# Kernel tuning notes

Measured on AMD Instinct MI355X. Metric: run time of the kernel, lower is better.

Reference implementation:

```python
import jax, jax.numpy as jnp
import numpy as np

B, N, D, H, IN, HID = 16, 1024, 256, 8, 256, 1024
HD = IN // H  # head dim = 32
EPS = 1e-5


def layer_norm(x, g, b):
    mu = jnp.mean(x, axis=-1, keepdims=True)
    var = jnp.var(x, axis=-1, keepdims=True)
    return (x - mu) / jnp.sqrt(var + EPS) * g + b


def setup_inputs() -> dict:
    key = jax.random.key(0)
    ks = jax.random.split(key, 12)
    s = 0.02
    return {
        "x": jax.random.normal(ks[0], (B, N, D), jnp.float32),
        "coords": jax.random.normal(ks[1], (B, N, 2), jnp.float32),
        "g1": jnp.ones((D,), jnp.float32),
        "b1": jnp.zeros((D,), jnp.float32),
        "Wqkv": jax.random.normal(ks[2], (3 * IN, D), jnp.float32) * s,
        "Wproj": jax.random.normal(ks[3], (IN, IN), jnp.float32) * s,
        "bproj": jnp.zeros((IN,), jnp.float32),
        "g2": jnp.ones((D,), jnp.float32),
        "b2": jnp.zeros((D,), jnp.float32),
        "W1": jax.random.normal(ks[4], (HID, D), jnp.float32) * s,
        "bb1": jnp.zeros((HID,), jnp.float32),
        "W2": jax.random.normal(ks[5], (D, HID), jnp.float32) * s,
        "bb2": jnp.zeros((D,), jnp.float32),
    }


def reference(x, coords, g1, b1, Wqkv, Wproj, bproj, g2, b2, W1, bb1, W2, bb2):
    # ---- Attention branch (pre-norm) ----
    h = layer_norm(x, g1, b1)                       # [B,N,D]
    qkv = h @ Wqkv.T                                # [B,N,3*IN]
    qkv = qkv.reshape(B, N, 3, H, HD).transpose(2, 0, 3, 1, 4)  # [3,B,H,N,HD]
    q, k, v = qkv[0], qkv[1], qkv[2]
    scale = HD ** -0.5
    attn = jnp.einsum('bhid,bhjd->bhij', q * scale, k)  # [B,H,N,N]
    attn = jax.nn.softmax(attn, axis=-1)
    o = jnp.einsum('bhij,bhjd->bhid', attn, v)      # [B,H,N,HD]
    o = o.transpose(0, 2, 1, 3).reshape(B, N, IN)   # [B,N,IN]
    o = o @ Wproj.T + bproj
    o = o + h                                       # residual inside Attention (vs normed input)
    x = x + o                                       # Block residual (double residual, faithful)
    # ---- MLP branch ----
    h2 = layer_norm(x, g2, b2)
    m = jax.nn.gelu(h2 @ W1.T + bb1, approximate=False) @ W2.T + bb2
    return x + m
```

## Files before the change

### kernel.cpp

```cpp
#include <hip/hip_runtime.h>
#include <hip/hip_bf16.h>
#include <math.h>

#define Bdim 16
#define Ndim 1024
#define Ddim 256
#define Hdim 8
#define HDdim 32
#define INdim 256
#define HIDdim 1024
#define Tdim (Bdim * Ndim)

typedef __attribute__((ext_vector_type(8)))  short bf16x8;
typedef __attribute__((ext_vector_type(4)))  short bf16x4;
typedef __attribute__((ext_vector_type(16))) float f32x16;
typedef unsigned int u32;

__device__ inline short f2bf(float x) {
    union { __hip_bfloat16 b; short s; } u;
    u.b = __float2bfloat16(x);
    return u.s;
}

__device__ inline float bf2f(short s) {
    return __uint_as_float(((u32)(unsigned short)s) << 16);
}

__device__ inline float fexp2(float x) {
#if __has_builtin(__builtin_amdgcn_exp2f)
    return __builtin_amdgcn_exp2f(x);
#else
    return exp2f(x);
#endif
}

__device__ inline u32 pack2bf(float a, float b) {
#if __has_builtin(__builtin_amdgcn_cvt_pk_bf16_f32)
    typedef __attribute__((ext_vector_type(2))) __bf16 bf16x2_t;
    union { bf16x2_t v; u32 u; } c;
    c.v = __builtin_amdgcn_cvt_pk_bf16_f32(a, b);
    return c.u;
#else
    u32 ua = __float_as_uint(a), ub = __float_as_uint(b);
    return ((ua + 0x8000u) >> 16) | ((ub + 0x8000u) & 0xffff0000u);
#endif
}

__device__ inline void plswap(u32 &a, u32 &b) {
    asm volatile("v_permlane32_swap_b32 %0, %1" : "+v"(a), "+v"(b));
}

__device__ inline float gelu_exact(float v) {
    return 0.5f * v * (1.0f + erff(v * 0.70710678118654752f));
}

#define N4_QKV  (3 * INdim * Ddim / 4)
#define N4_PROJ (INdim * INdim / 4)
#define N4_W1   (HIDdim * Ddim / 4)
#define N4_W2   (Ddim * HIDdim / 4)

__global__ __launch_bounds__(256) void cvt_all_kernel(const float* __restrict__ s0,
                                                      const float* __restrict__ s1,
                                                      const float* __restrict__ s2,
                                                      const float* __restrict__ s3,
                                                      short* __restrict__ d0,
                                                      short* __restrict__ d1,
                                                      short* __restrict__ d2,
                                                      short* __restrict__ d3) {
    int i = blockIdx.x * 256 + threadIdx.x;
    const float* src; short* dst; int j;
    if (i < N4_QKV)                          { src = s0; dst = d0; j = i; }
    else if (i < N4_QKV + N4_PROJ)           { src = s1; dst = d1; j = i - N4_QKV; }
    else if (i < N4_QKV + N4_PROJ + N4_W1)   { src = s2; dst = d2; j = i - N4_QKV - N4_PROJ; }
    else                                     { src = s3; dst = d3; j = i - N4_QKV - N4_PROJ - N4_W1; }
    float4 v = ((const float4*)src)[j];
    bf16x4 b;
    b[0] = f2bf(v.x); b[1] = f2bf(v.y); b[2] = f2bf(v.z); b[3] = f2bf(v.w);
    ((bf16x4*)dst)[j] = b;
}

__global__ __launch_bounds__(256) void ln4_kernel(const float* __restrict__ x,
                                                  const float* __restrict__ g,
                                                  const float* __restrict__ b,
                                                  float* __restrict__ outf,
                                                  short* __restrict__ outb) {
    int w = threadIdx.x >> 6, lane = threadIdx.x & 63;
    int row = blockIdx.x * 4 + w;
    float4 v = ((const float4*)x)[(size_t)row * 64 + lane];
    float s  = (v.x + v.y) + (v.z + v.w);
    float s2 = (v.x * v.x + v.y * v.y) + (v.z * v.z + v.w * v.w);
    #pragma unroll
    for (int off = 32; off; off >>= 1) {
        s  += __shfl_xor(s,  off, 64);
        s2 += __shfl_xor(s2, off, 64);
    }
    float mu   = s * (1.0f / Ddim);
    float var  = s2 * (1.0f / Ddim) - mu * mu;
    float rstd = rsqrtf(var + 1e-5f);
    float4 gg = ((const float4*)g)[lane];
    float4 bb = ((const float4*)b)[lane];
    float4 r;
    r.x = (v.x - mu) * rstd * gg.x + bb.x;
    r.y = (v.y - mu) * rstd * gg.y + bb.y;
    r.z = (v.z - mu) * rstd * gg.z + bb.z;
    r.w = (v.w - mu) * rstd * gg.w + bb.w;
    if (outf) ((float4*)outf)[(size_t)row * 64 + lane] = r;
    bf16x4 rb;
    rb[0] = f2bf(r.x); rb[1] = f2bf(r.y); rb[2] = f2bf(r.z); rb[3] = f2bf(r.w);
    ((bf16x4*)outb)[(size_t)row * 64 + lane] = rb;
}

#define EPI_NONE 0
#define EPI_PROJ 1
#define EPI_GELU 2
#define EPI_RES  3
#define EPI_QKV  4

#define GPAD64 72
#define SCALE2Q 0.25505654249892417f

template <int EPI, int BN>
__global__ __launch_bounds__(256) void gemm_mfma(const short* __restrict__ A,
                                                 const short* __restrict__ W,
                                                 void* __restrict__ Cv,
                                                 int M, int N, int K,
                                                 const float* __restrict__ bias,
                                                 const float* __restrict__ add1,
                                                 const float* __restrict__ add2) {
    __shared__ short As[128 * GPAD64];
    __shared__ short Bs[BN * GPAD64];
    const int tid = threadIdx.x, w = tid >> 6, lane = tid & 63;
    const int col = lane & 31;
    const int half_id = lane >> 5;
    const int m0 = blockIdx.y * 128, n0 = blockIdx.x * BN;
    const int wm = (BN == 128) ? (w & 1) * 64 : w * 32;
    const int wn = (BN == 128) ? (w >> 1) * 64 : 0;
    constexpr int TM = (BN == 128) ? 2 : 1;

    f32x16 acc[TM][2];
    #pragma unroll
    for (int i = 0; i < TM; ++i) { acc[i][0] = 0.0f; acc[i][1] = 0.0f; }

    const int sra = tid >> 1, ssa = (tid & 1) * 32;
    const int srb = (BN == 128) ? (tid >> 1) : (tid >> 2);
    const int ssb = (BN == 128) ? (tid & 1) * 32 : (tid & 3) * 16;
    constexpr int NB = (BN == 128) ? 4 : 2;

    const short* pAsrc = &A[(size_t)(m0 + sra) * K + ssa];
    const short* pBsrc = &W[(size_t)(n0 + srb) * K + ssb];

    bf16x8 pa[4], pb[NB];
    #pragma unroll
    for (int j = 0; j < 4; ++j) pa[j] = *(const bf16x8*)&pAsrc[j * 8];
    #pragma unroll
    for (int j = 0; j < NB; ++j) pb[j] = *(const bf16x8*)&pBsrc[j * 8];

    const int T = K >> 6;
    for (int kt = 0; kt < T; ++kt) {
        __syncthreads();
        #pragma unroll
        for (int j = 0; j < 4; ++j) *(bf16x8*)&As[sra * GPAD64 + ssa + j * 8] = pa[j];
        #pragma unroll
        for (int j = 0; j < NB; ++j) *(bf16x8*)&Bs[srb * GPAD64 + ssb + j * 8] = pb[j];
        __syncthreads();

        if (kt + 1 < T) {
            const short* a = pAsrc + (kt + 1) * 64;
            const short* b = pBsrc + (kt + 1) * 64;
            #pragma unroll
            for (int j = 0; j < 4; ++j) pa[j] = *(const bf16x8*)&a[j * 8];
            #pragma unroll
            for (int j = 0; j < NB; ++j) pb[j] = *(const bf16x8*)&b[j * 8];
        }

        #pragma unroll
        for (int ks = 0; ks < 4; ++ks) {
            bf16x8 af[TM], bfv[2];
            #pragma unroll
            for (int t = 0; t < TM; ++t)
                af[t] = *(const bf16x8*)&As[(wm + t * 32 + col) * GPAD64 + ks * 16 + half_id * 8];
            #pragma unroll
            for (int t = 0; t < 2; ++t)
                bfv[t] = *(const bf16x8*)&Bs[(wn + t * 32 + col) * GPAD64 + ks * 16 + half_id * 8];
            #pragma unroll
            for (int tm = 0; tm < TM; ++tm)
                #pragma unroll
                for (int tn = 0; tn < 2; ++tn)
                    acc[tm][tn] = __builtin_amdgcn_mfma_f32_32x32x16_bf16(
                        af[tm], bfv[tn], acc[tm][tn], 0, 0, 0);
        }
    }

    float* Cf = (float*)Cv;
    short* Cb = (short*)Cv;
    #pragma unroll
    for (int tm = 0; tm < TM; ++tm) {
        #pragma unroll
        for (int r = 0; r < 16; ++r) {
            int row = m0 + wm + tm * 32 + (r & 3) + 8 * (r >> 2) + 4 * half_id;
            #pragma unroll
            for (int tn = 0; tn < 2; ++tn) {
                int cn = n0 + wn + tn * 32 + col;
                size_t off = (size_t)row * N + cn;
                float v = acc[tm][tn][r];
                if (EPI != EPI_NONE && EPI != EPI_QKV) v += bias[cn];
                if (EPI == EPI_QKV && cn < 256) v *= SCALE2Q;
                if (EPI == EPI_GELU) v = gelu_exact(v);
                if (EPI == EPI_PROJ) v += add1[off] + add2[off];
                if (EPI == EPI_RES)  v += add1[off];
                if (EPI == EPI_PROJ || EPI == EPI_RES) Cf[off] = v;
                else                                   Cb[off] = f2bf(v);
            }
        }
    }
}

#define VTPAD 136

__global__ __launch_bounds__(256) void vtrans_kernel(const short* __restrict__ qkv,
                                                     short* __restrict__ vT) {
    __shared__ short Tl[32 * VTPAD];
    const int tid = threadIdx.x;
    const int bh = blockIdx.x, c = blockIdx.y;
    const int b = bh >> 3, head = bh & 7;
    {
        int r = tid >> 1, hv = tid & 1;
        const short* src = qkv + (size_t)b * Ndim * 768 + (size_t)(c * 128 + r) * 768
                           + 512 + head * 32 + hv * 16;
        bf16x8 v0 = *(const bf16x8*)&src[0];
        bf16x8 v1 = *(const bf16x8*)&src[8];
        #pragma unroll
        for (int i = 0; i < 8; ++i) {
            Tl[(hv * 16 + i) * VTPAD + r]     = v0[i];
            Tl[(hv * 16 + 8 + i) * VTPAD + r] = v1[i];
        }
    }
    __syncthreads();
    {
        int d = tid >> 3, j16 = (tid & 7) * 16;
        short* dst = vT + (size_t)(bh * 32 + d) * Ndim + c * 128 + j16;
        *(bf16x8*)&dst[0] = *(const bf16x8*)&Tl[d * VTPAD + j16];
        *(bf16x8*)&dst[8] = *(const bf16x8*)&Tl[d * VTPAD + j16 + 8];
    }
}

#define KVPAD 40
#define CHUNK 128

__global__ __launch_bounds__(256) void attn_mfma_kernel(const short* __restrict__ qkv,
                                                        const short* __restrict__ vT,
                                                        short* __restrict__ opart,
                                                        float* __restrict__ lpart) {
    __shared__ short Ks[CHUNK * KVPAD];
    __shared__ short Vt[32 * VTPAD];

    const int tid = threadIdx.x;
    const int w = tid >> 6;
    const int lane = tid & 63;
    const int col = lane & 31;
    const int half_id = lane >> 5;

    const int bh = blockIdx.y;
    const int b = bh >> 3, head = bh & 7;
    const int q0w = blockIdx.x * 128 + w * 32;
    const int part = blockIdx.z;

    const size_t qkvb = (size_t)b * Ndim * 768;
    short* op = opart + (size_t)part * Tdim * 256;
    float* lp = lpart + (size_t)part * Tdim * 8;

    const int sr = tid >> 1, shv = tid & 1;
    const short* ksrc = qkv + qkvb + (size_t)sr * 768 + 256 + head * 32 + shv * 16;
    const int sd = tid >> 3, sj16 = (tid & 7) * 16;
    const short* vsrc = vT + (size_t)(bh * 32 + sd) * Ndim + sj16;

    bf16x8 qf[2];
    {
        const short* qrow = qkv + qkvb + (size_t)(q0w + col) * 768 + head * 32;
        #pragma unroll
        for (int kh = 0; kh < 2; ++kh)
            qf[kh] = *(const bf16x8*)&qrow[kh * 16 + half_id * 8];
    }

    bf16x8 vone;
    #pragma unroll
    for (int i = 0; i < 8; ++i) vone[i] = (short)0x3F80;

    f32x16 o_acc = 0.0f, l_acc = 0.0f;

    const int c0 = part * 4;

    bf16x8 rk0, rk1, rv0, rv1;
    {
        const short* kp = ksrc + (size_t)(c0 * CHUNK) * 768;
        rk0 = *(const bf16x8*)&kp[0];
        rk1 = *(const bf16x8*)&kp[8];
        const short* vp = vsrc + c0 * CHUNK;
        rv0 = *(const bf16x8*)&vp[0];
        rv1 = *(const bf16x8*)&vp[8];
    }

    #pragma unroll
    for (int ci = 0; ci < 4; ++ci) {
        if (ci != 0) __syncthreads();
        *(bf16x8*)&Ks[sr * KVPAD + shv * 16]     = rk0;
        *(bf16x8*)&Ks[sr * KVPAD + shv * 16 + 8] = rk1;
        *(bf16x8*)&Vt[sd * VTPAD + sj16]     = rv0;
        *(bf16x8*)&Vt[sd * VTPAD + sj16 + 8] = rv1;
        __syncthreads();

        if (ci < 3) {
            const short* kp = ksrc + (size_t)((c0 + ci + 1) * CHUNK) * 768;
            rk0 = *(const bf16x8*)&kp[0];
            rk1 = *(const bf16x8*)&kp[8];
            const short* vp = vsrc + (c0 + ci + 1) * CHUNK;
            rv0 = *(const bf16x8*)&vp[0];
            rv1 = *(const bf16x8*)&vp[8];
        }

        f32x16 s_cur;
        {
            bf16x8 kf0 = *(bf16x8*)&Ks[col * KVPAD + half_id * 8];
            bf16x8 kf1 = *(bf16x8*)&Ks[col * KVPAD + 16 + half_id * 8];
            f32x16 z = 0.0f;
            z = __builtin_amdgcn_mfma_f32_32x32x16_bf16(kf0, qf[0], z, 0, 0, 0);
            z = __builtin_amdgcn_mfma_f32_32x32x16_bf16(kf1, qf[1], z, 0, 0, 0);
            s_cur = z;
        }
        #pragma unroll
        for (int jt = 0; jt < 4; ++jt) {
            f32x16 s_next;
            if (jt < 3) {
                bf16x8 kf0 = *(bf16x8*)&Ks[((jt + 1) * 32 + col) * KVPAD + half_id * 8];
                bf16x8 kf1 = *(bf16x8*)&Ks[((jt + 1) * 32 + col) * KVPAD + 16 + half_id * 8];
                f32x16 z = 0.0f;
                z = __builtin_amdgcn_mfma_f32_32x32x16_bf16(kf0, qf[0], z, 0, 0, 0);
                z = __builtin_amdgcn_mfma_f32_32x32x16_bf16(kf1, qf[1], z, 0, 0, 0);
                s_next = z;
            }

            bf16x8 vf0 = *(bf16x8*)&Vt[col * VTPAD + jt * 32 + half_id * 8];
            bf16x8 vf1 = *(bf16x8*)&Vt[col * VTPAD + jt * 32 + 16 + half_id * 8];

            u32 wd[8];
            #pragma unroll
            for (int g = 0; g < 8; ++g) {
                float e0 = fexp2(s_cur[2 * g + 0]);
                float e1 = fexp2(s_cur[2 * g + 1]);
                wd[g] = pack2bf(e0, e1);
            }
            plswap(wd[0], wd[2]); plswap(wd[1], wd[3]);
            plswap(wd[4], wd[6]); plswap(wd[5], wd[7]);

            union { u32 u[4]; bf16x8 v; } p0, p1;
            p0.u[0] = wd[0]; p0.u[1] = wd[1]; p0.u[2] = wd[2]; p0.u[3] = wd[3];
            p1.u[0] = wd[4]; p1.u[1] = wd[5]; p1.u[2] = wd[6]; p1.u[3] = wd[7];

            __builtin_amdgcn_s_setprio(1);
            o_acc = __builtin_amdgcn_mfma_f32_32x32x16_bf16(p0.v, vf0, o_acc, 0, 0, 0);
            o_acc = __builtin_amdgcn_mfma_f32_32x32x16_bf16(p1.v, vf1, o_acc, 0, 0, 0);
            l_acc = __builtin_amdgcn_mfma_f32_32x32x16_bf16(p0.v, vone, l_acc, 0, 0, 0);
            l_acc = __builtin_amdgcn_mfma_f32_32x32x16_bf16(p1.v, vone, l_acc, 0, 0, 0);
            __builtin_amdgcn_s_setprio(0);

            if (jt < 3) s_cur = s_next;
        }
    }

    #pragma unroll
    for (int r = 0; r < 16; ++r) {
        int q_r = (r & 3) + 8 * (r >> 2) + 4 * half_id;
        size_t gq = (size_t)(b * Ndim + q0w + q_r);
        op[gq * INdim + head * 32 + col] = f2bf(o_acc[r]);
    }
    if (col < 16) {
        int r = col;
        int q_r = (r & 3) + 8 * (r >> 2) + 4 * half_id;
        lp[(size_t)(b * Ndim + q0w + q_r) * 8 + head] = l_acc[r];
    }
}

__global__ __launch_bounds__(256) void combine_kernel(const short* __restrict__ opart,
                                                      const float* __restrict__ lpart,
                                                      short* __restrict__ oat) {
    int i = blockIdx.x * 256 + threadIdx.x;
    size_t base = (size_t)i * 8;
    int gq = (int)(base >> 8);
    int head = ((int)(base & 255)) >> 5;
    bf16x8 a = ((const bf16x8*)opart)[i];
    bf16x8 b = ((const bf16x8*)(opart + (size_t)Tdim * 256))[i];
    float l = lpart[(size_t)gq * 8 + head] + lpart[(size_t)Tdim * 8 + (size_t)gq * 8 + head];
    float rl = 1.0f / l;
    bf16x8 r;
    #pragma unroll
    for (int j = 0; j < 8; ++j) r[j] = f2bf((bf2f(a[j]) + bf2f(b[j])) * rl);
    ((bf16x8*)oat)[i] = r;
}

extern "C" void kernel_launch(void* const* d_in, const int* in_sizes, int n_in,
                              void* d_out, int out_size, void* d_ws, size_t ws_size,
                              hipStream_t stream) {
    const float* x     = (const float*)d_in[0];
    const float* g1    = (const float*)d_in[2];
    const float* b1    = (const float*)d_in[3];
    const float* Wqkv  = (const float*)d_in[4];
    const float* Wproj = (const float*)d_in[5];
    const float* bproj = (const float*)d_in[6];
    const float* g2    = (const float*)d_in[7];
    const float* b2    = (const float*)d_in[8];
    const float* W1    = (const float*)d_in[9];
    const float* bb1   = (const float*)d_in[10];
    const float* W2    = (const float*)d_in[11];
    const float* bb2   = (const float*)d_in[12];
    float* out = (float*)d_out;

    char* ws = (char*)d_ws;
    float* h      = (float*)(ws);
    short* h_bf   = (short*)(ws + (size_t)(16u << 20));
    short* qkv_bf = (short*)(ws + (size_t)(24u << 20));
    float* xnew   = (float*)(ws + (size_t)(24u << 20));
    short* oat_bf = (short*)(ws + (size_t)(40u << 20));
    short* opart  = (short*)(ws + (size_t)(48u << 20));
    short* mid_bf = (short*)(ws + (size_t)(48u << 20));
    float* lpart  = (float*)(ws + (size_t)(80u << 20));
    short* vT     = (short*)(ws + (size_t)(81u << 20));
    short* wqkv_b = (short*)(ws + (size_t)(89u << 20));
    short* wproj_b= (short*)(ws + (size_t)(89u << 20) + 768 * 1024);
    short* w1_b   = (short*)(ws + (size_t)(90u << 20));
    short* w2_b   = (short*)(ws + (size_t)(90u << 20) + 512 * 1024);

    cvt_all_kernel<<<(N4_QKV + N4_PROJ + N4_W1 + N4_W2 + 255) / 256, 256, 0, stream>>>(
        Wqkv, Wproj, W1, W2, wqkv_b, wproj_b, w1_b, w2_b);

    ln4_kernel<<<Tdim / 4, 256, 0, stream>>>(x, g1, b1, h, h_bf);
    gemm_mfma<EPI_QKV, 128><<<dim3(768 / 128, Tdim / 128), 256, 0, stream>>>(
        h_bf, wqkv_b, qkv_bf, Tdim, 768, 256, nullptr, nullptr, nullptr);
    vtrans_kernel<<<dim3(Bdim * Hdim, Ndim / 128), 256, 0, stream>>>(qkv_bf, vT);
    attn_mfma_kernel<<<dim3(Ndim / 128, Bdim * Hdim, 2), 256, 0, stream>>>(
        qkv_bf, vT, opart, lpart);
    combine_kernel<<<(Tdim * INdim / 8) / 256, 256, 0, stream>>>(opart, lpart, oat_bf);
    gemm_mfma<EPI_PROJ, 64><<<dim3(256 / 64, Tdim / 128), 256, 0, stream>>>(
        oat_bf, wproj_b, xnew, Tdim, 256, 256, bproj, h, x);
    ln4_kernel<<<Tdim / 4, 256, 0, stream>>>(xnew, g2, b2, nullptr, h_bf);
    gemm_mfma<EPI_GELU, 128><<<dim3(1024 / 128, Tdim / 128), 256, 0, stream>>>(
        h_bf, w1_b, mid_bf, Tdim, 1024, 256, bb1, nullptr, nullptr);
    gemm_mfma<EPI_RES, 64><<<dim3(256 / 64, Tdim / 128), 256, 0, stream>>>(
        mid_bf, w2_b, out, Tdim, 256, 1024, bb2, xnew, nullptr);
}
```

Baseline: 219.8 us.

## Shrink GEMM tiles to 64 rows and 32-wide K steps with block swizzle

The MFMA GEMM changes from 128-row tiles with K-step 64 to 64-row tiles with K-step 32, and the warp layout is reworked so each warp computes one 32-row slab. Launch grids double in the M dimension, and a block-index swizzle groups consecutive blocks into strided chunks to change the order in which tiles are visited. The aim is more blocks for occupancy and load balance across CUs and less LDS per block. In exchange, per-block data reuse drops, each warp issues fewer MFMAs per sync, and the K loop needs twice as many barriers.

```diff
diff --git a/kernel.cpp b/kernel.cpp
--- a/kernel.cpp
+++ b/kernel.cpp
@@ -116,7 +116,7 @@
 #define EPI_RES  3
 #define EPI_QKV  4
 
-#define GPAD64 72
+#define GPAD32 40
 #define SCALE2Q 0.25505654249892417f
 
 template <int EPI, int BN>
@@ -127,90 +127,85 @@
                                                  const float* __restrict__ bias,
                                                  const float* __restrict__ add1,
                                                  const float* __restrict__ add2) {
-    __shared__ short As[128 * GPAD64];
-    __shared__ short Bs[BN * GPAD64];
+    __shared__ short As[64 * GPAD32];
+    __shared__ short Bs[BN * GPAD32];
     const int tid = threadIdx.x, w = tid >> 6, lane = tid & 63;
     const int col = lane & 31;
     const int half_id = lane >> 5;
-    const int m0 = blockIdx.y * 128, n0 = blockIdx.x * BN;
-    const int wm = (BN == 128) ? (w & 1) * 64 : w * 32;
-    const int wn = (BN == 128) ? (w >> 1) * 64 : 0;
-    constexpr int TM = (BN == 128) ? 2 : 1;
-
-    f32x16 acc[TM][2];
-    #pragma unroll
-    for (int i = 0; i < TM; ++i) { acc[i][0] = 0.0f; acc[i][1] = 0.0f; }
-
-    const int sra = tid >> 1, ssa = (tid & 1) * 32;
+
+    const int nbx = gridDim.x;
+    const int flat = blockIdx.y * nbx + blockIdx.x;
+    const int cpx = (nbx * (int)gridDim.y) >> 3;
+    const int swz = (flat & 7) * cpx + (flat >> 3);
+    const int m0 = (swz / nbx) * 64, n0 = (swz % nbx) * BN;
+
+    const int wm = (w & 1) * 32;
+    const int wn = (BN == 128) ? (w >> 1) * 64 : (w >> 1) * 32;
+    constexpr int TN = (BN == 128) ? 2 : 1;
+
+    f32x16 acc[TN];
+    #pragma unroll
+    for (int t = 0; t < TN; ++t) acc[t] = 0.0f;
+
+    const int sra = tid >> 2, ssa = (tid & 3) * 8;
     const int srb = (BN == 128) ? (tid >> 1) : (tid >> 2);
-    const int ssb = (BN == 128) ? (tid & 1) * 32 : (tid & 3) * 16;
-    constexpr int NB = (BN == 128) ? 4 : 2;
+    const int ssb = (BN == 128) ? (tid & 1) * 16 : (tid & 3) * 8;
+    constexpr int NB = (BN == 128) ? 2 : 1;
 
     const short* pAsrc = &A[(size_t)(m0 + sra) * K + ssa];
     const short* pBsrc = &W[(size_t)(n0 + srb) * K + ssb];
 
-    bf16x8 pa[4], pb[NB];
-    #pragma unroll
-    for (int j = 0; j < 4; ++j) pa[j] = *(const bf16x8*)&pAsrc[j * 8];
+    bf16x8 pa, pb[NB];
+    pa = *(const bf16x8*)&pAsrc[0];
     #pragma unroll
     for (int j = 0; j < NB; ++j) pb[j] = *(const bf16x8*)&pBsrc[j * 8];
 
-    const int T = K >> 6;
+    const int T = K >> 5;
     for (int kt = 0; kt < T; ++kt) {
         __syncthreads();
-        #pragma unroll
-        for (int j = 0; j < 4; ++j) *(bf16x8*)&As[sra * GPAD64 + ssa + j * 8] = pa[j];
-        #pragma unroll
-        for (int j = 0; j < NB; ++j) *(bf16x8*)&Bs[srb * GPAD64 + ssb + j * 8] = pb[j];
+        *(bf16x8*)&As[sra * GPAD32 + ssa] = pa;
+        #pragma unroll
+        for (int j = 0; j < NB; ++j) *(bf16x8*)&Bs[srb * GPAD32 + ssb + j * 8] = pb[j];
         __syncthreads();
 
         if (kt + 1 < T) {
-            const short* a = pAsrc + (kt + 1) * 64;
-            const short* b = pBsrc + (kt + 1) * 64;
-            #pragma unroll
-            for (int j = 0; j < 4; ++j) pa[j] = *(const bf16x8*)&a[j * 8];
+            const short* a = pAsrc + (kt + 1) * 32;
+            const short* b = pBsrc + (kt + 1) * 32;
+            pa = *(const bf16x8*)&a[0];
             #pragma unroll
             for (int j = 0; j < NB; ++j) pb[j] = *(const bf16x8*)&b[j * 8];
         }
 
         #pragma unroll
-        for (int ks = 0; ks < 4; ++ks) {
-            bf16x8 af[TM], bfv[2];
+        for (int ks = 0; ks < 2; ++ks) {
+            bf16x8 af = *(const bf16x8*)&As[(wm + col) * GPAD32 + ks * 16 + half_id * 8];
+            bf16x8 bfv[TN];
             #pragma unroll
-            for (int t = 0; t < TM; ++t)
-                af[t] = *(const bf16x8*)&As[(wm + t * 32 + col) * GPAD64 + ks * 16 + half_id * 8];
+            for (int t = 0; t < TN; ++t)
+                bfv[t] = *(const bf16x8*)&Bs[(wn + t * 32 + col) * GPAD32 + ks * 16 + half_id * 8];
             #pragma unroll
-            for (int t = 0; t < 2; ++t)
-                bfv[t] = *(const bf16x8*)&Bs[(wn + t * 32 + col) * GPAD64 + ks * 16 + half_id * 8];
-            #pragma unroll
-            for (int tm = 0; tm < TM; ++tm)
-                #pragma unroll
-                for (int tn = 0; tn < 2; ++tn)
-                    acc[tm][tn] = __builtin_amdgcn_mfma_f32_32x32x16_bf16(
-                        af[tm], bfv[tn], acc[tm][tn], 0, 0, 0);
+            for (int t = 0; t < TN; ++t)
+                acc[t] = __builtin_amdgcn_mfma_f32_32x32x16_bf16(af, bfv[t], acc[t], 0, 0, 0);
         }
     }
 
     float* Cf = (float*)Cv;
     short* Cb = (short*)Cv;
     #pragma unroll
-    for (int tm = 0; tm < TM; ++tm) {
-        #pragma unroll
-        for (int r = 0; r < 16; ++r) {
-            int row = m0 + wm + tm * 32 + (r & 3) + 8 * (r >> 2) + 4 * half_id;
-            #pragma unroll
-            for (int tn = 0; tn < 2; ++tn) {
-                int cn = n0 + wn + tn * 32 + col;
-                size_t off = (size_t)row * N + cn;
-                float v = acc[tm][tn][r];
-                if (EPI != EPI_NONE && EPI != EPI_QKV) v += bias[cn];
-                if (EPI == EPI_QKV && cn < 256) v *= SCALE2Q;
-                if (EPI == EPI_GELU) v = gelu_exact(v);
-                if (EPI == EPI_PROJ) v += add1[off] + add2[off];
-                if (EPI == EPI_RES)  v += add1[off];
-                if (EPI == EPI_PROJ || EPI == EPI_RES) Cf[off] = v;
-                else                                   Cb[off] = f2bf(v);
-            }
+    for (int r = 0; r < 16; ++r) {
+        int row = m0 + wm + (r & 3) + 8 * (r >> 2) + 4 * half_id;
+        #pragma unroll
+        for (int t = 0; t < TN; ++t) {
+            int cn = n0 + wn + t * 32 + col;
+            size_t off = (size_t)row * N + cn;
+            float v = acc[t][r];
+            if (EPI != EPI_NONE && EPI != EPI_QKV) v += bias[cn];
+            if (EPI == EPI_QKV && cn < 256) v *= SCALE2Q;
+            if (EPI == EPI_GELU) v = gelu_exact(v);
+            if (EPI == EPI_PROJ) v += add1[off] + add2[off];
+            if (EPI == EPI_RES)  v += add1[off];
+            if (EPI == EPI_PROJ || EPI == EPI_RES) Cf[off] = v;
+            else                                   Cb[off] = f2bf(v);
         }
     }
 }
@@ -433,17 +428,17 @@
         Wqkv, Wproj, W1, W2, wqkv_b, wproj_b, w1_b, w2_b);
 
     ln4_kernel<<<Tdim / 4, 256, 0, stream>>>(x, g1, b1, h, h_bf);
-    gemm_mfma<EPI_QKV, 128><<<dim3(768 / 128, Tdim / 128), 256, 0, stream>>>(
+    gemm_mfma<EPI_QKV, 128><<<dim3(768 / 128, Tdim / 64), 256, 0, stream>>>(
         h_bf, wqkv_b, qkv_bf, Tdim, 768, 256, nullptr, nullptr, nullptr);
     vtrans_kernel<<<dim3(Bdim * Hdim, Ndim / 128), 256, 0, stream>>>(qkv_bf, vT);
     attn_mfma_kernel<<<dim3(Ndim / 128, Bdim * Hdim, 2), 256, 0, stream>>>(
         qkv_bf, vT, opart, lpart);
     combine_kernel<<<(Tdim * INdim / 8) / 256, 256, 0, stream>>>(opart, lpart, oat_bf);
-    gemm_mfma<EPI_PROJ, 64><<<dim3(256 / 64, Tdim / 128), 256, 0, stream>>>(
+    gemm_mfma<EPI_PROJ, 64><<<dim3(256 / 64, Tdim / 64), 256, 0, stream>>>(
         oat_bf, wproj_b, xnew, Tdim, 256, 256, bproj, h, x);
     ln4_kernel<<<Tdim / 4, 256, 0, stream>>>(xnew, g2, b2, nullptr, h_bf);
-    gemm_mfma<EPI_GELU, 128><<<dim3(1024 / 128, Tdim / 128), 256, 0, stream>>>(
+    gemm_mfma<EPI_GELU, 128><<<dim3(1024 / 128, Tdim / 64), 256, 0, stream>>>(
         h_bf, w1_b, mid_bf, Tdim, 1024, 256, bb1, nullptr, nullptr);
-    gemm_mfma<EPI_RES, 64><<<dim3(256 / 64, Tdim / 128), 256, 0, stream>>>(
+    gemm_mfma<EPI_RES, 64><<<dim3(256 / 64, Tdim / 64), 256, 0, stream>>>(
         mid_bf, w2_b, out, Tdim, 256, 1024, bb2, xnew, nullptr);
 }
```

Result: faster. 214.9 us (-2.2%).
